# Kernel tuning notes

Measured on AMD Instinct MI355X. Metric: run time of the kernel, lower is better.

The kernel has to match this reference:

```python
import jax, jax.numpy as jnp
import numpy as np

DEPTH, DIM, HEADS, HD, CTX, B = 4, 768, 12, 64, 2048, 4
INNER = HEADS * HD  # 768
EPS = 1e-5  # torch LayerNorm default


def _ln(x, g, b):
    m = jnp.mean(x, axis=-1, keepdims=True)
    v = jnp.var(x, axis=-1, keepdims=True)
    return (x - m) * jax.lax.rsqrt(v + EPS) * g + b


def setup_inputs() -> dict:
    key = jax.random.key(0)
    ks = jax.random.split(key, 12)
    s = 0.02
    return {
        "x": jax.random.normal(ks[0], (B, CTX, DIM), dtype=jnp.float32),
        "pos_emb": jax.random.normal(ks[1], (1, CTX, DIM), dtype=jnp.float32),
        # per-layer params stacked on leading depth axis
        "ln1_g": jnp.ones((DEPTH, DIM), jnp.float32),
        "ln1_b": jnp.zeros((DEPTH, DIM), jnp.float32),
        "Wq": jax.random.normal(ks[2], (DEPTH, DIM, INNER), dtype=jnp.float32) * s,
        "Wk": jax.random.normal(ks[3], (DEPTH, DIM, INNER), dtype=jnp.float32) * s,
        "Wv": jax.random.normal(ks[4], (DEPTH, DIM, INNER), dtype=jnp.float32) * s,
        "Wo": jax.random.normal(ks[5], (DEPTH, INNER, DIM), dtype=jnp.float32) * s,
        "ln2_g": jnp.ones((DEPTH, DIM), jnp.float32),
        "ln2_b": jnp.zeros((DEPTH, DIM), jnp.float32),
        "W1": jax.random.normal(ks[6], (DEPTH, DIM, DIM), dtype=jnp.float32) * s,  # hidden_dim == dim per source
        "b1": jnp.zeros((DEPTH, DIM), jnp.float32),
        "W2": jax.random.normal(ks[7], (DEPTH, DIM, DIM), dtype=jnp.float32) * s,
        "b2": jnp.zeros((DEPTH, DIM), jnp.float32),
    }


def reference(x, pos_emb, ln1_g, ln1_b, Wq, Wk, Wv, Wo, ln2_g, ln2_b, W1, b1, W2, b2):
    scale = 1.0 / np.sqrt(HD).astype(np.float32)
    x = x + pos_emb
    b, n, _ = x.shape
    for i in range(DEPTH):
        # --- attention block (pre-LN, residual) ---
        h = _ln(x, ln1_g[i], ln1_b[i])
        q = (h @ Wq[i]).reshape(b, n, HEADS, HD)
        k = (h @ Wk[i]).reshape(b, n, HEADS, HD)
        v = (h @ Wv[i]).reshape(b, n, HEADS, HD)
        scores = jnp.einsum('bihd,bjhd->bhij', q, k) * scale
        attn = jax.nn.softmax(scores, axis=-1)
        o = jnp.einsum('bhij,bjhd->bihd', attn, v).reshape(b, n, INNER)
        x = x + o @ Wo[i]
        # --- feed-forward block (LN -> Linear -> GELU -> Linear, residual) ---
        h = _ln(x, ln2_g[i], ln2_b[i])
        h = jax.nn.gelu(h @ W1[i] + b1[i], approximate=False)
        x = x + (h @ W2[i] + b2[i])
    return x
```

## Files before the change

kernel.cpp:

```cpp
#include <hip/hip_runtime.h>
#include <math.h>


#define DEPTH 4
#define DIM   768
#define HEADS 12
#define HD    64
#define CTXN  2048
#define BATCH 4
#define TOKENS (BATCH * CTXN)
#define QKVS  (3 * DIM)

typedef unsigned short u16;
typedef short s16x8 __attribute__((ext_vector_type(8)));
typedef float f32x4 __attribute__((ext_vector_type(4)));
typedef u16  u16x4 __attribute__((ext_vector_type(4)));

__device__ __forceinline__ u16 f2bf(float f) {
  union { float f; unsigned u; } c;
  c.f = f;
  unsigned u = c.u;
  return (u16)((u + 0x7FFFu + ((u >> 16) & 1u)) >> 16);
}

__device__ __forceinline__ u16 f2bf_fast(float f) {
  union { float f; unsigned u; } c;
  c.f = f;
  return (u16)((c.u + 0x8000u) >> 16);
}

__device__ __forceinline__ s16x8 ldfrag(const u16* t, int r, int g) {
  return *(const s16x8*)(t + r * 64 + 8 * (g ^ (r & 7)));
}
__device__ __forceinline__ void stfrag(u16* t, int r, int g, s16x8 v) {
  *(s16x8*)(t + r * 64 + 8 * (g ^ (r & 7))) = v;
}

__device__ __forceinline__ void gld_lds16(const u16* g, u16* l) {
#if __has_builtin(__builtin_amdgcn_global_load_lds)
  __builtin_amdgcn_global_load_lds(
      (const __attribute__((address_space(1))) unsigned int*)g,
      (__attribute__((address_space(3))) unsigned int*)l, 16, 0, 0);
#else
  int lane = threadIdx.x & 63;
  *(s16x8*)(l + lane * 8) = *(const s16x8*)(g);
#endif
}

__global__ __launch_bounds__(256) void add_pos_kernel(
    const float* __restrict__ X, const float* __restrict__ P,
    float* __restrict__ Y, int n, int pn) {
  int i = blockIdx.x * 256 + threadIdx.x;
  if (i < n) Y[i] = X[i] + P[i % pn];
}

__global__ __launch_bounds__(256) void wconv_kernel(
    const float* __restrict__ Wq, const float* __restrict__ Wk,
    const float* __restrict__ Wv, const float* __restrict__ Wo,
    const float* __restrict__ W1, const float* __restrict__ W2,
    u16* __restrict__ dst) {
  int mat = blockIdx.z;
  int layer = mat / 6, type = mat % 6;
  const float* srcs[6] = {Wq, Wk, Wv, Wo, W1, W2};
  const float* src = srcs[type] + (size_t)layer * DIM * DIM;
  u16* d = dst + (size_t)mat * DIM * DIM;
  __shared__ float L[32][33];
  int k0 = blockIdx.y * 32, n0 = blockIdx.x * 32;
  int r = threadIdx.x >> 3, c4 = (threadIdx.x & 7) * 4;
  float4 v = *(const float4*)&src[(size_t)(k0 + r) * DIM + n0 + c4];
  L[c4 + 0][r] = v.x; L[c4 + 1][r] = v.y;
  L[c4 + 2][r] = v.z; L[c4 + 3][r] = v.w;
  __syncthreads();
  u16x4 w;
#pragma unroll
  for (int j = 0; j < 4; ++j) w[j] = f2bf(L[r][c4 + j]);
  *(u16x4*)&d[(size_t)(n0 + r) * DIM + k0 + c4] = w;
}

__global__ __launch_bounds__(256) void ln_kernel(
    const float* __restrict__ X, const float* __restrict__ g,
    const float* __restrict__ b, u16* __restrict__ Y) {
  int t = blockIdx.x;
  int tid = threadIdx.x;
  const float* xr = X + (size_t)t * DIM;
  float v0 = xr[tid], v1 = xr[tid + 256], v2 = xr[tid + 512];
  float s = v0 + v1 + v2;
  float q = v0 * v0 + v1 * v1 + v2 * v2;
#pragma unroll
  for (int o = 32; o > 0; o >>= 1) {
    s += __shfl_xor(s, o);
    q += __shfl_xor(q, o);
  }
  __shared__ float rs[4], rq[4];
  int w = tid >> 6;
  if ((tid & 63) == 0) { rs[w] = s; rq[w] = q; }
  __syncthreads();
  s = rs[0] + rs[1] + rs[2] + rs[3];
  q = rq[0] + rq[1] + rq[2] + rq[3];
  float mean = s * (1.0f / DIM);
  float var  = q * (1.0f / DIM) - mean * mean;
  float r = rsqrtf(var + 1e-5f);
  u16* yr = Y + (size_t)t * DIM;
  yr[tid]       = f2bf((v0 - mean) * r * g[tid]       + b[tid]);
  yr[tid + 256] = f2bf((v1 - mean) * r * g[tid + 256] + b[tid + 256]);
  yr[tid + 512] = f2bf((v2 - mean) * r * g[tid + 512] + b[tid + 512]);
}

template <int BM, int HAS_BIAS, int HAS_GELU, int HAS_RES, int OUT_BF16>
__global__ __launch_bounds__(256, 3) void gemm_bf16(
    const u16* __restrict__ A, const u16* __restrict__ Bt,
    const float* __restrict__ bias, void* __restrict__ Cv, int Nc) {
  constexpr int MI = BM / 32;
  float* C = (float*)Cv;
  u16* Cb = (u16*)Cv;
  __shared__ __align__(16) u16 As[BM * 64];
  __shared__ __align__(16) u16 Bs[128 * 64];
  int tid = threadIdx.x;
  int wave = tid >> 6, lane = tid & 63, ln = lane & 15, quad = lane >> 4;
  int wr = wave >> 1, wc = wave & 1;

  int nwg = gridDim.x * gridDim.y;
  int lin = blockIdx.y * gridDim.x + blockIdx.x;
  int swz = (lin & 7) * (nwg >> 3) + (lin >> 3);
  int bx = swz % gridDim.x, by = swz / gridDim.x;
  int m0 = by * BM, n0 = bx * 128;

  int sg = (lane & 7) ^ ((lane >> 3) & 7);
  int srowA = wave * (BM / 4) + (lane >> 3);
  int srowB = wave * 32 + (lane >> 3);
  const u16* ga = A + (size_t)(m0 + srowA) * DIM + sg * 8;
  const u16* gb = Bt + (size_t)(n0 + srowB) * DIM + sg * 8;
  u16* la = As + wave * (BM / 4) * 64;
  u16* lb = Bs + wave * 2048;

  f32x4 acc[MI][4];
  const f32x4 zero = {0.0f, 0.0f, 0.0f, 0.0f};
#pragma unroll
  for (int i = 0; i < MI; ++i)
#pragma unroll
    for (int j = 0; j < 4; ++j) acc[i][j] = zero;

  for (int kt = 0; kt < DIM / 64; ++kt) {
#pragma unroll
    for (int i = 0; i < MI; ++i)
      gld_lds16(ga + (size_t)i * 8 * DIM, la + i * 512);
#pragma unroll
    for (int i = 0; i < 4; ++i)
      gld_lds16(gb + (size_t)i * 8 * DIM, lb + i * 512);
    ga += 64; gb += 64;
    __syncthreads();

    s16x8 bfr0[4], bfr1[4];
#pragma unroll
    for (int ni = 0; ni < 4; ++ni) {
      bfr0[ni] = ldfrag(Bs, wc * 64 + ni * 16 + ln, quad);
      bfr1[ni] = ldfrag(Bs, wc * 64 + ni * 16 + ln, 4 + quad);
    }
#pragma unroll
    for (int mi = 0; mi < MI; ++mi) {
      s16x8 a0 = ldfrag(As, wr * (BM / 2) + mi * 16 + ln, quad);
      s16x8 a1 = ldfrag(As, wr * (BM / 2) + mi * 16 + ln, 4 + quad);
#pragma unroll
      for (int ni = 0; ni < 4; ++ni) {
        acc[mi][ni] = __builtin_amdgcn_mfma_f32_16x16x32_bf16(a0, bfr0[ni], acc[mi][ni], 0, 0, 0);
        acc[mi][ni] = __builtin_amdgcn_mfma_f32_16x16x32_bf16(a1, bfr1[ni], acc[mi][ni], 0, 0, 0);
      }
    }
    __syncthreads();
  }

#pragma unroll
  for (int ni = 0; ni < 4; ++ni) {
    int c = n0 + wc * 64 + ni * 16 + ln;
    float bv = HAS_BIAS ? bias[c] : 0.0f;
#pragma unroll
    for (int mi = 0; mi < MI; ++mi) {
#pragma unroll
      for (int reg = 0; reg < 4; ++reg) {
        int r = m0 + wr * (BM / 2) + mi * 16 + quad * 4 + reg;
        float v = acc[mi][ni][reg] + bv;
        if (HAS_GELU) v = 0.5f * v * (1.0f + erff(v * 0.70710678118654752f));
        size_t o = (size_t)r * Nc + c;
        if (OUT_BF16) { Cb[o] = f2bf(v); }
        else if (HAS_RES) { C[o] += v; }
        else { C[o] = v; }
      }
    }
  }
}

__global__ __launch_bounds__(256) void vtrans_kernel(
    const u16* __restrict__ QKV, u16* __restrict__ Vt) {
  int bid = blockIdx.x;
  int tt = bid & 31;
  int h  = (bid >> 5) % HEADS;
  int b  = bid / (32 * HEADS);
  int tid = threadIdx.x;
  __shared__ u16 T[64][66];
  const u16* src = QKV + ((size_t)(b * CTXN + tt * 64)) * QKVS + 2 * DIM + h * HD;
#pragma unroll
  for (int i = 0; i < 2; ++i) {
    int idx = tid + i * 256, r = idx >> 3, g = idx & 7;
    s16x8 v = *(const s16x8*)&src[(size_t)r * QKVS + g * 8];
#pragma unroll
    for (int j = 0; j < 8; ++j) T[g * 8 + j][r] = (u16)v[j];
  }
  __syncthreads();
#pragma unroll
  for (int i = 0; i < 2; ++i) {
    int idx = tid + i * 256, d = idx >> 3, g = idx & 7;
    s16x8 w;
#pragma unroll
    for (int j = 0; j < 8; ++j) w[j] = (short)T[d][g * 8 + j];
    *(s16x8*)&Vt[((size_t)(b * HEADS + h) * HD + d) * CTXN + tt * 64 + g * 8] = w;
  }
}

__global__ __launch_bounds__(256) void attn_kernel(
    const u16* __restrict__ QKV, const u16* __restrict__ Vt,
    u16* __restrict__ Ob) {
  const int tiles = CTXN / 64;
  const int nblk = BATCH * HEADS * tiles;
  int orig = blockIdx.x;
  int bid = (orig & 7) * (nblk >> 3) + (orig >> 3);
  int qt = bid % tiles;
  int h  = (bid / tiles) % HEADS;
  int b  = bid / (tiles * HEADS);
  int tid = threadIdx.x;
  int wave = tid >> 6, lane = tid & 63, ln = lane & 15, quad = lane >> 4;

  __shared__ __align__(16) char smem[24576];
  u16* Ks = (u16*)smem;
  u16* Vs = (u16*)(smem + 8192);
  u16* Ps = (u16*)(smem + 16384);
  float (*Of)[65] = (float (*)[65])smem;

  const u16* qrow =
      QKV + ((size_t)(b * CTXN + qt * 64 + wave * 16 + ln)) * QKVS + h * HD;
  s16x8 aq0 = *(const s16x8*)&qrow[quad * 8];
  s16x8 aq1 = *(const s16x8*)&qrow[32 + quad * 8];

  float m = -1e30f, l = 0.0f;
  f32x4 oacc[4];
  const f32x4 zero = {0.0f, 0.0f, 0.0f, 0.0f};
#pragma unroll
  for (int i = 0; i < 4; ++i) oacc[i] = zero;

  const u16* kb0 = QKV + ((size_t)b * CTXN) * QKVS + DIM + h * HD;
  const u16* vt0 = Vt + ((size_t)(b * HEADS + h) * HD) * CTXN;
  const float lg = 0.125f * 1.4426950408889634f;
  const float THR = 44.3614195f;

  int sr0 = tid >> 3, sg0 = tid & 7;
  int sr1 = sr0 + 32;
  const u16* kp0 = kb0 + (size_t)sr0 * QKVS + sg0 * 8;
  const u16* kp1 = kb0 + (size_t)sr1 * QKVS + sg0 * 8;
  const u16* vp0 = vt0 + (size_t)sr0 * CTXN + sg0 * 8;
  const u16* vp1 = vt0 + (size_t)sr1 * CTXN + sg0 * 8;

  s16x8 rk0 = *(const s16x8*)kp0;
  s16x8 rk1 = *(const s16x8*)kp1;
  s16x8 rv0 = *(const s16x8*)vp0;
  s16x8 rv1 = *(const s16x8*)vp1;

  for (int kt = 0; kt < tiles; ++kt) {
    stfrag(Ks, sr0, sg0, rk0);
    stfrag(Ks, sr1, sg0, rk1);
    stfrag(Vs, sr0, sg0, rv0);
    stfrag(Vs, sr1, sg0, rv1);
    __syncthreads();

    {
      int ktn = (kt + 1 < tiles) ? kt + 1 : kt;
      rk0 = *(const s16x8*)(kp0 + (size_t)ktn * 64 * QKVS);
      rk1 = *(const s16x8*)(kp1 + (size_t)ktn * 64 * QKVS);
      rv0 = *(const s16x8*)(vp0 + (size_t)ktn * 64);
      rv1 = *(const s16x8*)(vp1 + (size_t)ktn * 64);
    }

    f32x4 sacc[4];
    __builtin_amdgcn_s_setprio(1);
#pragma unroll
    for (int nb = 0; nb < 4; ++nb) {
      sacc[nb] = zero;
      s16x8 k0 = ldfrag(Ks, nb * 16 + ln, quad);
      s16x8 k1 = ldfrag(Ks, nb * 16 + ln, 4 + quad);
      sacc[nb] = __builtin_amdgcn_mfma_f32_16x16x32_bf16(k0, aq0, sacc[nb], 0, 0, 0);
      sacc[nb] = __builtin_amdgcn_mfma_f32_16x16x32_bf16(k1, aq1, sacc[nb], 0, 0, 0);
    }
    __builtin_amdgcn_s_setprio(0);

    float mx = fmaxf(fmaxf(sacc[0][0], sacc[0][1]), fmaxf(sacc[0][2], sacc[0][3]));
#pragma unroll
    for (int nb = 1; nb < 4; ++nb)
      mx = fmaxf(mx, fmaxf(fmaxf(sacc[nb][0], sacc[nb][1]),
                           fmaxf(sacc[nb][2], sacc[nb][3])));
    mx = fmaxf(mx, __shfl_xor(mx, 16));
    mx = fmaxf(mx, __shfl_xor(mx, 32));

    if (!__all(mx <= m + THR)) {
      float mnew = fmaxf(m, mx);
      float alpha = exp2f((m - mnew) * lg);
      float ar[4];
#pragma unroll
      for (int reg = 0; reg < 4; ++reg) ar[reg] = __shfl(alpha, quad * 4 + reg);
#pragma unroll
      for (int nb = 0; nb < 4; ++nb)
#pragma unroll
        for (int reg = 0; reg < 4; ++reg) oacc[nb][reg] *= ar[reg];
      l *= alpha;
      m = mnew;
    }

    float nm = -m * lg;
    float ls = 0.0f;
    u16x4 pk[4];
#pragma unroll
    for (int nb = 0; nb < 4; ++nb) {
#pragma unroll
      for (int reg = 0; reg < 4; ++reg) {
        float p = exp2f(fmaf(sacc[nb][reg], lg, nm));
        ls += p;
        pk[nb][reg] = f2bf_fast(p);
      }
    }
    ls += __shfl_xor(ls, 16);
    ls += __shfl_xor(ls, 32);
    l += ls;

    {
      int row = wave * 16 + ln;
      int rs = row & 7;
      int half = (quad & 1) * 4;
#pragma unroll
      for (int nb = 0; nb < 4; ++nb) {
        int g0 = nb * 2 + (quad >> 1);
        *(u16x4*)&Ps[row * 64 + 8 * (g0 ^ rs) + half] = pk[nb];
      }
    }
    __syncthreads();

    s16x8 ap0 = ldfrag(Ps, wave * 16 + ln, quad);
    s16x8 ap1 = ldfrag(Ps, wave * 16 + ln, 4 + quad);
    __builtin_amdgcn_s_setprio(1);
#pragma unroll
    for (int nb = 0; nb < 4; ++nb) {
      s16x8 bv0 = ldfrag(Vs, nb * 16 + ln, quad);
      s16x8 bv1 = ldfrag(Vs, nb * 16 + ln, 4 + quad);
      oacc[nb] = __builtin_amdgcn_mfma_f32_16x16x32_bf16(ap0, bv0, oacc[nb], 0, 0, 0);
      oacc[nb] = __builtin_amdgcn_mfma_f32_16x16x32_bf16(ap1, bv1, oacc[nb], 0, 0, 0);
    }
    __builtin_amdgcn_s_setprio(0);
    __syncthreads();
  }

  float li[4];
#pragma unroll
  for (int reg = 0; reg < 4; ++reg) li[reg] = 1.0f / __shfl(l, quad * 4 + reg);

#pragma unroll
  for (int nb = 0; nb < 4; ++nb)
#pragma unroll
    for (int reg = 0; reg < 4; ++reg)
      Of[wave * 16 + quad * 4 + reg][nb * 16 + ln] = oacc[nb][reg] * li[reg];
  __syncthreads();
  {
    int r = tid >> 2, c0 = (tid & 3) * 16;
    u16* dst = Ob + ((size_t)(b * CTXN + qt * 64 + r)) * DIM + h * HD + c0;
#pragma unroll
    for (int k = 0; k < 4; ++k) {
      u16x4 w;
#pragma unroll
      for (int j = 0; j < 4; ++j) w[j] = f2bf(Of[r][c0 + 4 * k + j]);
      *(u16x4*)&dst[4 * k] = w;
    }
  }
}

extern "C" void kernel_launch(void* const* d_in, const int* in_sizes, int n_in,
                              void* d_out, int out_size, void* d_ws, size_t ws_size,
                              hipStream_t stream) {
  const float* x_in  = (const float*)d_in[0];
  const float* pos   = (const float*)d_in[1];
  const float* ln1_g = (const float*)d_in[2];
  const float* ln1_b = (const float*)d_in[3];
  const float* Wq    = (const float*)d_in[4];
  const float* Wk    = (const float*)d_in[5];
  const float* Wv    = (const float*)d_in[6];
  const float* Wo    = (const float*)d_in[7];
  const float* ln2_g = (const float*)d_in[8];
  const float* ln2_b = (const float*)d_in[9];
  const float* W1    = (const float*)d_in[10];
  const float* b1    = (const float*)d_in[11];
  const float* W2    = (const float*)d_in[12];
  const float* b2    = (const float*)d_in[13];

  float* x = (float*)d_out;
  const size_t TD = (size_t)TOKENS * DIM;
  u16* hb  = (u16*)d_ws;
  u16* qkv = hb + TD;
  u16* vt  = qkv + 3 * TD;
  u16* wt  = vt + TD;
  u16* fb  = qkv;

  int n = (int)TD, pn = CTXN * DIM;
  add_pos_kernel<<<(n + 255) / 256, 256, 0, stream>>>(x_in, pos, x, n, pn);
  {
    dim3 wg(24, 24, 24);
    wconv_kernel<<<wg, 256, 0, stream>>>(Wq, Wk, Wv, Wo, W1, W2, wt);
  }

  const size_t WSZ = (size_t)DIM * DIM;
  dim3 gq(QKVS / 128, TOKENS / 128);
  dim3 gg(DIM / 128, TOKENS / 64);
  int nblk_attn = BATCH * HEADS * (CTXN / 64);
  for (int i = 0; i < DEPTH; ++i) {
    const u16* wqkv = wt + (size_t)(i * 6 + 0) * WSZ;
    const u16* wo   = wt + (size_t)(i * 6 + 3) * WSZ;
    const u16* w1   = wt + (size_t)(i * 6 + 4) * WSZ;
    const u16* w2   = wt + (size_t)(i * 6 + 5) * WSZ;

    ln_kernel<<<TOKENS, 256, 0, stream>>>(x, ln1_g + i * DIM, ln1_b + i * DIM, hb);
    gemm_bf16<128,0,0,0,1><<<gq, 256, 0, stream>>>(hb, wqkv, nullptr, qkv, QKVS);
    vtrans_kernel<<<nblk_attn, 256, 0, stream>>>(qkv, vt);
    attn_kernel<<<nblk_attn, 256, 0, stream>>>(qkv, vt, hb);
    gemm_bf16<64,0,0,1,0><<<gg, 256, 0, stream>>>(hb, wo, nullptr, x, DIM);

    ln_kernel<<<TOKENS, 256, 0, stream>>>(x, ln2_g + i * DIM, ln2_b + i * DIM, hb);
    gemm_bf16<64,1,1,0,1><<<gg, 256, 0, stream>>>(hb, w1, b1 + i * DIM, fb, DIM);
    gemm_bf16<64,1,0,1,0><<<gg, 256, 0, stream>>>(fb, w2, b2 + i * DIM, x, DIM);
  }
}
```

Measured before the change: 1.041 ms.

## Double-buffer GEMM LDS tiles and shrink QKV GEMM row tile

```diff
diff --git a/kernel.cpp b/kernel.cpp
--- a/kernel.cpp
+++ b/kernel.cpp
@@ -111,10 +111,13 @@
     const u16* __restrict__ A, const u16* __restrict__ Bt,
     const float* __restrict__ bias, void* __restrict__ Cv, int Nc) {
   constexpr int MI = BM / 32;
+  constexpr int ASZ = BM * 64;
+  constexpr int BSZ = 128 * 64;
+  constexpr int KSTEPS = DIM / 64;
   float* C = (float*)Cv;
   u16* Cb = (u16*)Cv;
-  __shared__ __align__(16) u16 As[BM * 64];
-  __shared__ __align__(16) u16 Bs[128 * 64];
+  __shared__ __align__(16) u16 As[2 * ASZ];
+  __shared__ __align__(16) u16 Bs[2 * BSZ];
   int tid = threadIdx.x;
   int wave = tid >> 6, lane = tid & 63, ln = lane & 15, quad = lane >> 4;
   int wr = wave >> 1, wc = wave & 1;
@@ -133,6 +136,19 @@
   u16* la = As + wave * (BM / 4) * 64;
   u16* lb = Bs + wave * 2048;
 
+  auto STAGE = [&](int kt, int buf) {
+    const u16* a = ga + kt * 64;
+    const u16* b = gb + kt * 64;
+    u16* lA = la + buf * ASZ;
+    u16* lB = lb + buf * BSZ;
+#pragma unroll
+    for (int i = 0; i < MI; ++i)
+      gld_lds16(a + (size_t)i * 8 * DIM, lA + i * 512);
+#pragma unroll
+    for (int i = 0; i < 4; ++i)
+      gld_lds16(b + (size_t)i * 8 * DIM, lB + i * 512);
+  };
+
   f32x4 acc[MI][4];
   const f32x4 zero = {0.0f, 0.0f, 0.0f, 0.0f};
 #pragma unroll
@@ -140,26 +156,25 @@
 #pragma unroll
     for (int j = 0; j < 4; ++j) acc[i][j] = zero;
 
-  for (int kt = 0; kt < DIM / 64; ++kt) {
-#pragma unroll
-    for (int i = 0; i < MI; ++i)
-      gld_lds16(ga + (size_t)i * 8 * DIM, la + i * 512);
-#pragma unroll
-    for (int i = 0; i < 4; ++i)
-      gld_lds16(gb + (size_t)i * 8 * DIM, lb + i * 512);
-    ga += 64; gb += 64;
-    __syncthreads();
-
+  STAGE(0, 0);
+  __syncthreads();
+
+  for (int kt = 0; kt < KSTEPS; ++kt) {
+    int cur = kt & 1;
+    if (kt + 1 < KSTEPS) STAGE(kt + 1, cur ^ 1);
+
+    const u16* AsC = As + cur * ASZ;
+    const u16* BsC = Bs + cur * BSZ;
     s16x8 bfr0[4], bfr1[4];
 #pragma unroll
     for (int ni = 0; ni < 4; ++ni) {
-      bfr0[ni] = ldfrag(Bs, wc * 64 + ni * 16 + ln, quad);
-      bfr1[ni] = ldfrag(Bs, wc * 64 + ni * 16 + ln, 4 + quad);
+      bfr0[ni] = ldfrag(BsC, wc * 64 + ni * 16 + ln, quad);
+      bfr1[ni] = ldfrag(BsC, wc * 64 + ni * 16 + ln, 4 + quad);
     }
 #pragma unroll
     for (int mi = 0; mi < MI; ++mi) {
-      s16x8 a0 = ldfrag(As, wr * (BM / 2) + mi * 16 + ln, quad);
-      s16x8 a1 = ldfrag(As, wr * (BM / 2) + mi * 16 + ln, 4 + quad);
+      s16x8 a0 = ldfrag(AsC, wr * (BM / 2) + mi * 16 + ln, quad);
+      s16x8 a1 = ldfrag(AsC, wr * (BM / 2) + mi * 16 + ln, 4 + quad);
 #pragma unroll
       for (int ni = 0; ni < 4; ++ni) {
         acc[mi][ni] = __builtin_amdgcn_mfma_f32_16x16x32_bf16(a0, bfr0[ni], acc[mi][ni], 0, 0, 0);
@@ -411,7 +426,7 @@
   }
 
   const size_t WSZ = (size_t)DIM * DIM;
-  dim3 gq(QKVS / 128, TOKENS / 128);
+  dim3 gq(QKVS / 128, TOKENS / 64);
   dim3 gg(DIM / 128, TOKENS / 64);
   int nblk_attn = BATCH * HEADS * (CTXN / 64);
   for (int i = 0; i < DEPTH; ++i) {
@@ -421,7 +436,7 @@
     const u16* w2   = wt + (size_t)(i * 6 + 5) * WSZ;
 
     ln_kernel<<<TOKENS, 256, 0, stream>>>(x, ln1_g + i * DIM, ln1_b + i * DIM, hb);
-    gemm_bf16<128,0,0,0,1><<<gq, 256, 0, stream>>>(hb, wqkv, nullptr, qkv, QKVS);
+    gemm_bf16<64,0,0,0,1><<<gq, 256, 0, stream>>>(hb, wqkv, nullptr, qkv, QKVS);
     vtrans_kernel<<<nblk_attn, 256, 0, stream>>>(qkv, vt);
     attn_kernel<<<nblk_attn, 256, 0, stream>>>(qkv, vt, hb);
     gemm_bf16<64,0,0,1,0><<<gg, 256, 0, stream>>>(hb, wo, nullptr, x, DIM);
```

After: 1.111 ms. +6.7%, slower.

## Process 128 query rows per attention block to reuse each K/V tile

Applied to the files above, without the earlier changes.

```diff
diff --git a/kernel.cpp b/kernel.cpp
--- a/kernel.cpp
+++ b/kernel.cpp
@@ -220,31 +220,35 @@
     const u16* __restrict__ QKV, const u16* __restrict__ Vt,
     u16* __restrict__ Ob) {
   const int tiles = CTXN / 64;
-  const int nblk = BATCH * HEADS * tiles;
+  const int qtiles = CTXN / 128;
+  const int nblk = BATCH * HEADS * qtiles;
   int orig = blockIdx.x;
   int bid = (orig & 7) * (nblk >> 3) + (orig >> 3);
-  int qt = bid % tiles;
-  int h  = (bid / tiles) % HEADS;
-  int b  = bid / (tiles * HEADS);
+  int qt = bid % qtiles;
+  int h  = (bid / qtiles) % HEADS;
+  int b  = bid / (qtiles * HEADS);
   int tid = threadIdx.x;
   int wave = tid >> 6, lane = tid & 63, ln = lane & 15, quad = lane >> 4;
 
-  __shared__ __align__(16) char smem[24576];
+  __shared__ __align__(16) char smem[32768];
   u16* Ks = (u16*)smem;
   u16* Vs = (u16*)(smem + 8192);
   u16* Ps = (u16*)(smem + 16384);
   float (*Of)[65] = (float (*)[65])smem;
 
-  const u16* qrow =
-      QKV + ((size_t)(b * CTXN + qt * 64 + wave * 16 + ln)) * QKVS + h * HD;
-  s16x8 aq0 = *(const s16x8*)&qrow[quad * 8];
-  s16x8 aq1 = *(const s16x8*)&qrow[32 + quad * 8];
-
-  float m = -1e30f, l = 0.0f;
-  f32x4 oacc[4];
+  const u16* qrowA =
+      QKV + ((size_t)(b * CTXN + qt * 128 + wave * 16 + ln)) * QKVS + h * HD;
+  const u16* qrowB = qrowA + (size_t)64 * QKVS;
+  s16x8 aq0 = *(const s16x8*)&qrowA[quad * 8];
+  s16x8 aq1 = *(const s16x8*)&qrowA[32 + quad * 8];
+  s16x8 aq2 = *(const s16x8*)&qrowB[quad * 8];
+  s16x8 aq3 = *(const s16x8*)&qrowB[32 + quad * 8];
+
+  float mA = -1e30f, lA = 0.0f, mB = -1e30f, lB = 0.0f;
+  f32x4 oA[4], oB[4];
   const f32x4 zero = {0.0f, 0.0f, 0.0f, 0.0f};
 #pragma unroll
-  for (int i = 0; i < 4; ++i) oacc[i] = zero;
+  for (int i = 0; i < 4; ++i) { oA[i] = zero; oB[i] = zero; }
 
   const u16* kb0 = QKV + ((size_t)b * CTXN) * QKVS + DIM + h * HD;
   const u16* vt0 = Vt + ((size_t)(b * HEADS + h) * HD) * CTXN;
@@ -263,6 +267,8 @@
   s16x8 rv0 = *(const s16x8*)vp0;
   s16x8 rv1 = *(const s16x8*)vp1;
 
+  int rowA = wave * 16 + ln, rowB = rowA + 64;
+
   for (int kt = 0; kt < tiles; ++kt) {
     stfrag(Ks, sr0, sg0, rk0);
     stfrag(Ks, sr1, sg0, rk1);
@@ -278,95 +284,143 @@
       rv1 = *(const s16x8*)(vp1 + (size_t)ktn * 64);
     }
 
-    f32x4 sacc[4];
+    f32x4 sA[4], sB[4];
     __builtin_amdgcn_s_setprio(1);
 #pragma unroll
     for (int nb = 0; nb < 4; ++nb) {
-      sacc[nb] = zero;
       s16x8 k0 = ldfrag(Ks, nb * 16 + ln, quad);
       s16x8 k1 = ldfrag(Ks, nb * 16 + ln, 4 + quad);
-      sacc[nb] = __builtin_amdgcn_mfma_f32_16x16x32_bf16(k0, aq0, sacc[nb], 0, 0, 0);
-      sacc[nb] = __builtin_amdgcn_mfma_f32_16x16x32_bf16(k1, aq1, sacc[nb], 0, 0, 0);
+      sA[nb] = __builtin_amdgcn_mfma_f32_16x16x32_bf16(k0, aq0, zero, 0, 0, 0);
+      sA[nb] = __builtin_amdgcn_mfma_f32_16x16x32_bf16(k1, aq1, sA[nb], 0, 0, 0);
+      sB[nb] = __builtin_amdgcn_mfma_f32_16x16x32_bf16(k0, aq2, zero, 0, 0, 0);
+      sB[nb] = __builtin_amdgcn_mfma_f32_16x16x32_bf16(k1, aq3, sB[nb], 0, 0, 0);
     }
     __builtin_amdgcn_s_setprio(0);
 
-    float mx = fmaxf(fmaxf(sacc[0][0], sacc[0][1]), fmaxf(sacc[0][2], sacc[0][3]));
-#pragma unroll
-    for (int nb = 1; nb < 4; ++nb)
-      mx = fmaxf(mx, fmaxf(fmaxf(sacc[nb][0], sacc[nb][1]),
-                           fmaxf(sacc[nb][2], sacc[nb][3])));
-    mx = fmaxf(mx, __shfl_xor(mx, 16));
-    mx = fmaxf(mx, __shfl_xor(mx, 32));
-
-    if (!__all(mx <= m + THR)) {
-      float mnew = fmaxf(m, mx);
-      float alpha = exp2f((m - mnew) * lg);
+    float mxA = fmaxf(fmaxf(sA[0][0], sA[0][1]), sA[0][2]);
+    float mxB = fmaxf(fmaxf(sB[0][0], sB[0][1]), sB[0][2]);
+#pragma unroll
+    for (int nb = 0; nb < 4; ++nb)
+#pragma unroll
+      for (int reg = (nb == 0 ? 3 : 0); reg < 4; ++reg) {
+        mxA = fmaxf(mxA, sA[nb][reg]);
+        mxB = fmaxf(mxB, sB[nb][reg]);
+      }
+    mxA = fmaxf(mxA, __shfl_xor(mxA, 16));
+    mxA = fmaxf(mxA, __shfl_xor(mxA, 32));
+    mxB = fmaxf(mxB, __shfl_xor(mxB, 16));
+    mxB = fmaxf(mxB, __shfl_xor(mxB, 32));
+
+    if (!__all(mxA <= mA + THR)) {
+      float mnew = fmaxf(mA, mxA);
+      float alpha = exp2f((mA - mnew) * lg);
       float ar[4];
 #pragma unroll
       for (int reg = 0; reg < 4; ++reg) ar[reg] = __shfl(alpha, quad * 4 + reg);
 #pragma unroll
       for (int nb = 0; nb < 4; ++nb)
 #pragma unroll
-        for (int reg = 0; reg < 4; ++reg) oacc[nb][reg] *= ar[reg];
-      l *= alpha;
-      m = mnew;
-    }
-
-    float nm = -m * lg;
-    float ls = 0.0f;
-    u16x4 pk[4];
+        for (int reg = 0; reg < 4; ++reg) oA[nb][reg] *= ar[reg];
+      lA *= alpha;
+      mA = mnew;
+    }
+    if (!__all(mxB <= mB + THR)) {
+      float mnew = fmaxf(mB, mxB);
+      float alpha = exp2f((mB - mnew) * lg);
+      float ar[4];
+#pragma unroll
+      for (int reg = 0; reg < 4; ++reg) ar[reg] = __shfl(alpha, quad * 4 + reg);
+#pragma unroll
+      for (int nb = 0; nb < 4; ++nb)
+#pragma unroll
+        for (int reg = 0; reg < 4; ++reg) oB[nb][reg] *= ar[reg];
+      lB *= alpha;
+      mB = mnew;
+    }
+
+    float nmA = -mA * lg, nmB = -mB * lg;
+    float lsA = 0.0f, lsB = 0.0f;
+    u16x4 pkA[4], pkB[4];
 #pragma unroll
     for (int nb = 0; nb < 4; ++nb) {
 #pragma unroll
       for (int reg = 0; reg < 4; ++reg) {
-        float p = exp2f(fmaf(sacc[nb][reg], lg, nm));
-        ls += p;
-        pk[nb][reg] = f2bf_fast(p);
+        float pA = exp2f(fmaf(sA[nb][reg], lg, nmA));
+        float pB = exp2f(fmaf(sB[nb][reg], lg, nmB));
+        lsA += pA; lsB += pB;
+        pkA[nb][reg] = f2bf_fast(pA);
+        pkB[nb][reg] = f2bf_fast(pB);
       }
     }
-    ls += __shfl_xor(ls, 16);
-    ls += __shfl_xor(ls, 32);
-    l += ls;
+    lsA += __shfl_xor(lsA, 16);
+    lsA += __shfl_xor(lsA, 32);
+    lsB += __shfl_xor(lsB, 16);
+    lsB += __shfl_xor(lsB, 32);
+    lA += lsA; lB += lsB;
 
     {
-      int row = wave * 16 + ln;
-      int rs = row & 7;
+      int rs = rowA & 7;
       int half = (quad & 1) * 4;
 #pragma unroll
       for (int nb = 0; nb < 4; ++nb) {
         int g0 = nb * 2 + (quad >> 1);
-        *(u16x4*)&Ps[row * 64 + 8 * (g0 ^ rs) + half] = pk[nb];
+        *(u16x4*)&Ps[rowA * 64 + 8 * (g0 ^ rs) + half] = pkA[nb];
+        *(u16x4*)&Ps[rowB * 64 + 8 * (g0 ^ rs) + half] = pkB[nb];
       }
     }
-    __syncthreads();
-
-    s16x8 ap0 = ldfrag(Ps, wave * 16 + ln, quad);
-    s16x8 ap1 = ldfrag(Ps, wave * 16 + ln, 4 + quad);
+
+    s16x8 apA0 = ldfrag(Ps, rowA, quad);
+    s16x8 apA1 = ldfrag(Ps, rowA, 4 + quad);
+    s16x8 apB0 = ldfrag(Ps, rowB, quad);
+    s16x8 apB1 = ldfrag(Ps, rowB, 4 + quad);
     __builtin_amdgcn_s_setprio(1);
 #pragma unroll
     for (int nb = 0; nb < 4; ++nb) {
       s16x8 bv0 = ldfrag(Vs, nb * 16 + ln, quad);
       s16x8 bv1 = ldfrag(Vs, nb * 16 + ln, 4 + quad);
-      oacc[nb] = __builtin_amdgcn_mfma_f32_16x16x32_bf16(ap0, bv0, oacc[nb], 0, 0, 0);
-      oacc[nb] = __builtin_amdgcn_mfma_f32_16x16x32_bf16(ap1, bv1, oacc[nb], 0, 0, 0);
+      oA[nb] = __builtin_amdgcn_mfma_f32_16x16x32_bf16(apA0, bv0, oA[nb], 0, 0, 0);
+      oA[nb] = __builtin_amdgcn_mfma_f32_16x16x32_bf16(apA1, bv1, oA[nb], 0, 0, 0);
+      oB[nb] = __builtin_amdgcn_mfma_f32_16x16x32_bf16(apB0, bv0, oB[nb], 0, 0, 0);
+      oB[nb] = __builtin_amdgcn_mfma_f32_16x16x32_bf16(apB1, bv1, oB[nb], 0, 0, 0);
     }
     __builtin_amdgcn_s_setprio(0);
     __syncthreads();
   }
 
-  float li[4];
-#pragma unroll
-  for (int reg = 0; reg < 4; ++reg) li[reg] = 1.0f / __shfl(l, quad * 4 + reg);
+  float liA[4], liB[4];
+#pragma unroll
+  for (int reg = 0; reg < 4; ++reg) {
+    liA[reg] = 1.0f / __shfl(lA, quad * 4 + reg);
+    liB[reg] = 1.0f / __shfl(lB, quad * 4 + reg);
+  }
 
 #pragma unroll
   for (int nb = 0; nb < 4; ++nb)
 #pragma unroll
     for (int reg = 0; reg < 4; ++reg)
-      Of[wave * 16 + quad * 4 + reg][nb * 16 + ln] = oacc[nb][reg] * li[reg];
+      Of[wave * 16 + quad * 4 + reg][nb * 16 + ln] = oA[nb][reg] * liA[reg];
   __syncthreads();
   {
     int r = tid >> 2, c0 = (tid & 3) * 16;
-    u16* dst = Ob + ((size_t)(b * CTXN + qt * 64 + r)) * DIM + h * HD + c0;
+    u16* dst = Ob + ((size_t)(b * CTXN + qt * 128 + r)) * DIM + h * HD + c0;
+#pragma unroll
+    for (int k = 0; k < 4; ++k) {
+      u16x4 w;
+#pragma unroll
+      for (int j = 0; j < 4; ++j) w[j] = f2bf(Of[r][c0 + 4 * k + j]);
+      *(u16x4*)&dst[4 * k] = w;
+    }
+  }
+  __syncthreads();
+#pragma unroll
+  for (int nb = 0; nb < 4; ++nb)
+#pragma unroll
+    for (int reg = 0; reg < 4; ++reg)
+      Of[wave * 16 + quad * 4 + reg][nb * 16 + ln] = oB[nb][reg] * liB[reg];
+  __syncthreads();
+  {
+    int r = tid >> 2, c0 = (tid & 3) * 16;
+    u16* dst = Ob + ((size_t)(b * CTXN + qt * 128 + 64 + r)) * DIM + h * HD + c0;
 #pragma unroll
     for (int k = 0; k < 4; ++k) {
       u16x4 w;
@@ -413,7 +467,8 @@
   const size_t WSZ = (size_t)DIM * DIM;
   dim3 gq(QKVS / 128, TOKENS / 128);
   dim3 gg(DIM / 128, TOKENS / 64);
-  int nblk_attn = BATCH * HEADS * (CTXN / 64);
+  int nblk_vt = BATCH * HEADS * (CTXN / 64);
+  int nblk_attn = BATCH * HEADS * (CTXN / 128);
   for (int i = 0; i < DEPTH; ++i) {
     const u16* wqkv = wt + (size_t)(i * 6 + 0) * WSZ;
     const u16* wo   = wt + (size_t)(i * 6 + 3) * WSZ;
@@ -422,7 +477,7 @@
 
     ln_kernel<<<TOKENS, 256, 0, stream>>>(x, ln1_g + i * DIM, ln1_b + i * DIM, hb);
     gemm_bf16<128,0,0,0,1><<<gq, 256, 0, stream>>>(hb, wqkv, nullptr, qkv, QKVS);
-    vtrans_kernel<<<nblk_attn, 256, 0, stream>>>(qkv, vt);
+    vtrans_kernel<<<nblk_vt, 256, 0, stream>>>(qkv, vt);
     attn_kernel<<<nblk_attn, 256, 0, stream>>>(qkv, vt, hb);
     gemm_bf16<64,0,0,1,0><<<gg, 256, 0, stream>>>(hb, wo, nullptr, x, DIM);
 
```

New measurement: 1.152 ms. 10.7% more time.
